# Optimization experiments

Measured on AMD Instinct MI355X. Metric: run time of the kernel, lower is better.

## Reference

```python
import jax, jax.numpy as jnp
import numpy as np

INPUT_DIM = 512
HIDDEN_DIM = 1024
OUTPUT_DIM = 1000
BATCH = 256
SEQ_LEN = 256


def setup_inputs() -> dict:
    key = jax.random.key(0)
    ks = jax.random.split(key, 7)
    std = 1.0 / np.sqrt(HIDDEN_DIM)
    u = lambda k, shape: jax.random.uniform(k, shape, jnp.float32, -std, std)
    return {
        "x": jax.random.normal(ks[0], (BATCH, SEQ_LEN, INPUT_DIM), jnp.float32),
        "w_x2h": u(ks[1], (4 * HIDDEN_DIM, INPUT_DIM)),
        "b_x2h": u(ks[2], (4 * HIDDEN_DIM,)),
        "w_h2h": u(ks[3], (4 * HIDDEN_DIM, HIDDEN_DIM)),
        "b_h2h": u(ks[4], (4 * HIDDEN_DIM,)),
        "w_fc": u(ks[5], (OUTPUT_DIM, HIDDEN_DIM)),
        "b_fc": u(ks[6], (OUTPUT_DIM,)),
    }


def _lstm_last_hidden(x, w_x2h, b_x2h, w_h2h, b_h2h):
    B, T, D = x.shape
    H = w_h2h.shape[1]
    # Precompute input-to-hidden for all timesteps in one big GEMM: [B,T,4H]
    xg = jnp.einsum("btd,gd->btg", x, w_x2h) + b_x2h + b_h2h
    xg = jnp.swapaxes(xg, 0, 1)  # [T,B,4H] for scan

    def step(carry, xg_t):
        h, c = carry
        gates = xg_t + h @ w_h2h.T  # [B,4H]
        i, f, g, o = jnp.split(gates, 4, axis=1)
        i = jax.nn.sigmoid(i)
        f = jax.nn.sigmoid(f)
        g = jnp.tanh(g)
        o = jax.nn.sigmoid(o)
        c = c * f + i * g
        h = o * jnp.tanh(c)
        return (h, c), None

    h0 = jnp.zeros((B, H), x.dtype)
    c0 = jnp.zeros((B, H), x.dtype)
    (h_last, _), _ = jax.lax.scan(step, (h0, c0), xg)
    return h_last


def reference(x, w_x2h, b_x2h, w_h2h, b_h2h, w_fc, b_fc):
    h_last = _lstm_last_hidden(x, w_x2h, b_x2h, w_h2h, b_h2h)  # [B,H]
    return h_last @ w_fc.T + b_fc  # [B,OUTPUT_DIM]
```

## Files before the change

kernel.cpp:

```cpp
#include <hip/hip_runtime.h>

typedef __attribute__((ext_vector_type(8))) short short8;
typedef __attribute__((ext_vector_type(4))) float floatx4;

#define DIN  512
#define HSZ  1024
#define G4   4096
#define KTOT 1536
#define BQ   256
#define TT   256

#define MFMA __builtin_amdgcn_mfma_f32_16x16x32_bf16

__device__ __forceinline__ unsigned short f2bf(float f){
  unsigned int u = __float_as_uint(f);
  u += 0x7fffu + ((u >> 16) & 1u);
  return (unsigned short)(u >> 16);
}
__device__ __forceinline__ unsigned int pack2(float a, float b){
  return (unsigned int)f2bf(a) | ((unsigned int)f2bf(b) << 16);
}

__global__ void prep_wcat(const float* __restrict__ wx, const float* __restrict__ wh,
                          const float* __restrict__ bx, const float* __restrict__ bh,
                          unsigned short* __restrict__ Wcat, float* __restrict__ bias){
  int gid = blockIdx.x * blockDim.x + threadIdx.x;
  int idx = gid * 8;
  int g = idx / KTOT;
  int k = idx - g * KTOT;
  const float* src = (k < DIN) ? (wx + (size_t)g * DIN + k)
                               : (wh + (size_t)g * HSZ + (k - DIN));
  float4 f0 = *(const float4*)(src);
  float4 f1 = *(const float4*)(src + 4);
  uint4 v = make_uint4(pack2(f0.x,f0.y), pack2(f0.z,f0.w), pack2(f1.x,f1.y), pack2(f1.z,f1.w));
  *(uint4*)(Wcat + (size_t)g * KTOT + k) = v;
  if (gid < G4) bias[gid] = bx[gid] + bh[gid];
}

__global__ void prep_wfc(const float* __restrict__ wfc, unsigned short* __restrict__ Wfcb){
  int gid = blockIdx.x * blockDim.x + threadIdx.x;
  int idx = gid * 8;
  int n = idx >> 10;
  int k = idx & 1023;
  uint4 v;
  if (n < 1000){
    const float* src = wfc + (size_t)n * 1024 + k;
    float4 f0 = *(const float4*)(src);
    float4 f1 = *(const float4*)(src + 4);
    v = make_uint4(pack2(f0.x,f0.y), pack2(f0.z,f0.w), pack2(f1.x,f1.y), pack2(f1.z,f1.w));
  } else {
    v = make_uint4(0u, 0u, 0u, 0u);
  }
  *(uint4*)(Wfcb + idx) = v;
}

__global__ void prep_x(const float* __restrict__ x, unsigned short* __restrict__ xbf){
  int gid = blockIdx.x * 256 + threadIdx.x;
  int d8 = gid & 63;
  int b  = (gid >> 6) & 255;
  int t  = gid >> 14;
  const float* src = x + (((size_t)b * TT) + t) * DIN + d8 * 8;
  float4 f0 = *(const float4*)(src);
  float4 f1 = *(const float4*)(src + 4);
  uint4 v = make_uint4(pack2(f0.x,f0.y), pack2(f0.z,f0.w), pack2(f1.x,f1.y), pack2(f1.z,f1.w));
  *(uint4*)(xbf + (((size_t)t * BQ) + b) * DIN + d8 * 8) = v;
}

__global__ void init_misc(unsigned int* __restrict__ h0w, unsigned int* __restrict__ cnt, int ncnt){
  int gid = blockIdx.x * 256 + threadIdx.x;
  if (gid < 131072) h0w[gid] = 0u;
  if (gid < ncnt)   cnt[gid] = 0u;
}

__global__ __launch_bounds__(512, 2)
void lstm_persist(const unsigned short* __restrict__ xbf,
                  const unsigned short* __restrict__ Wcat,
                  const float* __restrict__ bias,
                  unsigned short* __restrict__ hseq,
                  unsigned int* __restrict__ cnt){
  extern __shared__ char smem[];
  char*  Ws  = smem;
  float* Gt2 = (float*)(smem + 98304);
  float* Bls = (float*)(smem + 98304 + 34816);

  const int tid  = threadIdx.x;
  const int bx   = blockIdx.x;
  const int bg   = bx >> 7;
  const int b0   = bg << 7;
  const int u0   = (bx & 127) << 3;
  const int lane = tid & 63;
  const int w    = tid >> 6;
  const int rg   = w & 3;
  const int kg   = w >> 2;

  {
    int c  = tid >> 4;
    int ch = tid & 15;
    int g  = c >> 3, j = c & 7;
    const char* src = (const char*)(Wcat + (size_t)(g * HSZ + u0 + j) * KTOT);
    char* dst = Ws + c * 3072;
    int xr = j << 4;
    #pragma unroll
    for (int q = 0; q < 12; ++q){
      int k2 = ch * 192 + q * 16;
      *(uint4*)(dst + (k2 ^ xr)) = *(const uint4*)(src + k2);
    }
    if (tid < 32) Bls[tid] = bias[(size_t)(tid >> 3) * HSZ + u0 + (tid & 7)];
  }
  __syncthreads();

  const int kq8  = (lane >> 4) * 8;
  const int cA   = lane & 15;
  const int cB   = 16 + (lane & 15);
  const char* bpA = Ws + cA * 3072; const int xorA = (cA & 7) << 4;
  const char* bpB = Ws + cB * 3072; const int xorB = (cB & 7) << 4;

  const size_t rowA0 = (size_t)(b0 + rg * 32 + (lane & 15));

  const int erow = tid >> 2;
  const int eup  = (tid & 3) * 2;
  float cst0 = 0.f, cst1 = 0.f;

  for (int t = 0; t < TT; ++t){
    const unsigned short* hin  = hseq + (size_t)t * (BQ * HSZ);
    unsigned short*       hout = hseq + (size_t)(t + 1) * (BQ * HSZ);

    floatx4 acc[2][2][2];
    #pragma unroll
    for (int ab = 0; ab < 2; ++ab)
      #pragma unroll
      for (int rf = 0; rf < 2; ++rf)
        #pragma unroll
        for (int cf = 0; cf < 2; ++cf)
          acc[ab][rf][cf] = (floatx4){0.f,0.f,0.f,0.f};

    {
      const unsigned short* xr0 = xbf + ((size_t)t * BQ + rowA0) * DIN + kg * 256 + kq8;
      const unsigned short* xr1 = xr0 + (size_t)16 * DIN;
      const int bbase = kg * 512 + kq8 * 2;
      short8 a[4][2], b[4][2];
      #pragma unroll
      for (int p = 0; p < 4; ++p){
        a[p][0] = *(const short8*)(xr0 + p * 32);
        a[p][1] = *(const short8*)(xr1 + p * 32);
        int bb = bbase + p * 64;
        b[p][0] = *(const short8*)(bpA + (bb ^ xorA));
        b[p][1] = *(const short8*)(bpB + (bb ^ xorB));
      }
      #pragma unroll
      for (int j = 0; j < 8; ++j){
        int sl = j & 3, ab = j & 1;
        acc[ab][0][0] = MFMA(a[sl][0], b[sl][0], acc[ab][0][0], 0, 0, 0);
        acc[ab][0][1] = MFMA(a[sl][0], b[sl][1], acc[ab][0][1], 0, 0, 0);
        acc[ab][1][0] = MFMA(a[sl][1], b[sl][0], acc[ab][1][0], 0, 0, 0);
        acc[ab][1][1] = MFMA(a[sl][1], b[sl][1], acc[ab][1][1], 0, 0, 0);
        if (j < 4){
          int jj = j + 4;
          a[sl][0] = *(const short8*)(xr0 + jj * 32);
          a[sl][1] = *(const short8*)(xr1 + jj * 32);
          int bb = bbase + jj * 64;
          b[sl][0] = *(const short8*)(bpA + (bb ^ xorA));
          b[sl][1] = *(const short8*)(bpB + (bb ^ xorB));
        }
      }
    }

    if (t > 0){
      if (tid == 0){
        const unsigned int* cp = &cnt[((size_t)t * 2 + bg) * 32];
        while (__hip_atomic_load(cp, __ATOMIC_RELAXED, __HIP_MEMORY_SCOPE_AGENT) < 128u)
          __builtin_amdgcn_s_sleep(1);
      }
      __syncthreads();
      asm volatile("" ::: "memory");
    }

    {
      const unsigned short* hr0 = hin + rowA0 * HSZ + kg * 512 + kq8;
      const unsigned short* hr1 = hr0 + (size_t)16 * HSZ;
      const int bbase = 1024 + kg * 1024 + kq8 * 2;
      short8 a[4][2], b[4][2];
      #pragma unroll
      for (int p = 0; p < 4; ++p){
        a[p][0] = *(const short8*)(hr0 + p * 32);
        a[p][1] = *(const short8*)(hr1 + p * 32);
        int bb = bbase + p * 64;
        b[p][0] = *(const short8*)(bpA + (bb ^ xorA));
        b[p][1] = *(const short8*)(bpB + (bb ^ xorB));
      }
      #pragma unroll
      for (int j = 0; j < 16; ++j){
        int sl = j & 3, ab = j & 1;
        acc[ab][0][0] = MFMA(a[sl][0], b[sl][0], acc[ab][0][0], 0, 0, 0);
        acc[ab][0][1] = MFMA(a[sl][0], b[sl][1], acc[ab][0][1], 0, 0, 0);
        acc[ab][1][0] = MFMA(a[sl][1], b[sl][0], acc[ab][1][0], 0, 0, 0);
        acc[ab][1][1] = MFMA(a[sl][1], b[sl][1], acc[ab][1][1], 0, 0, 0);
        if (j < 12){
          int jj = j + 4;
          a[sl][0] = *(const short8*)(hr0 + jj * 32);
          a[sl][1] = *(const short8*)(hr1 + jj * 32);
          int bb = bbase + jj * 64;
          b[sl][0] = *(const short8*)(bpA + (bb ^ xorA));
          b[sl][1] = *(const short8*)(bpB + (bb ^ xorB));
        }
      }
    }

    {
      float* gdst = Gt2 + kg * (128 * 34);
      int r0 = rg * 32 + (lane >> 4) * 4;
      #pragma unroll
      for (int rf = 0; rf < 2; ++rf){
        floatx4 g0 = acc[0][rf][0] + acc[1][rf][0];
        floatx4 g1 = acc[0][rf][1] + acc[1][rf][1];
        #pragma unroll
        for (int r = 0; r < 4; ++r){
          gdst[(r0 + rf * 16 + r) * 34 + cA] = g0[r];
          gdst[(r0 + rf * 16 + r) * 34 + cB] = g1[r];
        }
      }
    }
    __syncthreads();

    {
      const float* g0p = Gt2 + erow * 34;
      const float* g1p = g0p + 128 * 34;
      float gi0 = g0p[     eup] + g1p[     eup] + Bls[     eup];
      float gf0 = g0p[ 8 + eup] + g1p[ 8 + eup] + Bls[ 8 + eup];
      float gg0 = g0p[16 + eup] + g1p[16 + eup] + Bls[16 + eup];
      float go0 = g0p[24 + eup] + g1p[24 + eup] + Bls[24 + eup];
      float gi1 = g0p[     eup + 1] + g1p[     eup + 1] + Bls[     eup + 1];
      float gf1 = g0p[ 8 + eup + 1] + g1p[ 8 + eup + 1] + Bls[ 8 + eup + 1];
      float gg1 = g0p[16 + eup + 1] + g1p[16 + eup + 1] + Bls[16 + eup + 1];
      float go1 = g0p[24 + eup + 1] + g1p[24 + eup + 1] + Bls[24 + eup + 1];

      float iv0 = 1.f / (1.f + __expf(-gi0));
      float fv0 = 1.f / (1.f + __expf(-gf0));
      float e20 = __expf(-2.f * fmaxf(fminf(gg0, 30.f), -30.f));
      float gv0 = (1.f - e20) / (1.f + e20);
      float ov0 = 1.f / (1.f + __expf(-go0));
      float cn0 = cst0 * fv0 + iv0 * gv0;
      cst0 = cn0;
      float ec0 = __expf(-2.f * fmaxf(fminf(cn0, 30.f), -30.f));
      float hv0 = ov0 * (1.f - ec0) / (1.f + ec0);

      float iv1 = 1.f / (1.f + __expf(-gi1));
      float fv1 = 1.f / (1.f + __expf(-gf1));
      float e21 = __expf(-2.f * fmaxf(fminf(gg1, 30.f), -30.f));
      float gv1 = (1.f - e21) / (1.f + e21);
      float ov1 = 1.f / (1.f + __expf(-go1));
      float cn1 = cst1 * fv1 + iv1 * gv1;
      cst1 = cn1;
      float ec1 = __expf(-2.f * fmaxf(fminf(cn1, 30.f), -30.f));
      float hv1 = ov1 * (1.f - ec1) / (1.f + ec1);

      __hip_atomic_store((unsigned int*)(hout + (size_t)(b0 + erow) * HSZ + u0 + eup),
                         pack2(hv0, hv1), __ATOMIC_RELAXED, __HIP_MEMORY_SCOPE_AGENT);
    }
    __syncthreads();

    if (tid == 0){
      __hip_atomic_fetch_add(&cnt[((size_t)(t + 1) * 2 + bg) * 32], 1u,
                             __ATOMIC_RELAXED, __HIP_MEMORY_SCOPE_AGENT);
    }
  }
}

__global__ __launch_bounds__(256, 1)
void fc_kernel(const unsigned short* __restrict__ h, const unsigned short* __restrict__ wfc,
               const float* __restrict__ bfc, float* __restrict__ out){
  int bx = blockIdx.x, tid = threadIdx.x;
  int wave = tid >> 6, lane = tid & 63;
  int row0 = (bx >> 4) * 64 + wave * 16;
  int col0 = (bx & 15) * 64;
  int lr = lane & 15, lk = (lane >> 4) * 8;
  floatx4 acc[4] = {{0.f,0.f,0.f,0.f},{0.f,0.f,0.f,0.f},{0.f,0.f,0.f,0.f},{0.f,0.f,0.f,0.f}};
  #pragma unroll 4
  for (int ks = 0; ks < 32; ++ks){
    int k = ks * 32 + lk;
    short8 a = *(const short8*)(h + (size_t)(row0 + lr) * 1024 + k);
    #pragma unroll
    for (int fj = 0; fj < 4; ++fj){
      short8 b = *(const short8*)(wfc + (size_t)(col0 + fj * 16 + lr) * 1024 + k);
      acc[fj] = MFMA(a, b, acc[fj], 0, 0, 0);
    }
  }
  #pragma unroll
  for (int fj = 0; fj < 4; ++fj){
    int col = col0 + fj * 16 + lr;
    if (col < 1000){
      #pragma unroll
      for (int r = 0; r < 4; ++r){
        int row = row0 + (lane >> 4) * 4 + r;
        out[(size_t)row * 1000 + col] = acc[fj][r] + bfc[col];
      }
    }
  }
}

extern "C" void kernel_launch(void* const* d_in, const int* in_sizes, int n_in,
                              void* d_out, int out_size, void* d_ws, size_t ws_size,
                              hipStream_t stream){
  const float* x    = (const float*)d_in[0];
  const float* wx2h = (const float*)d_in[1];
  const float* bx2h = (const float*)d_in[2];
  const float* wh2h = (const float*)d_in[3];
  const float* bh2h = (const float*)d_in[4];
  const float* wfc  = (const float*)d_in[5];
  const float* bfc  = (const float*)d_in[6];
  float* out = (float*)d_out;
  char* ws = (char*)d_ws;

  unsigned short* Wcat = (unsigned short*)(ws + 0);
  unsigned short* Wfcb = (unsigned short*)(ws + 12582912);
  float*          bias = (float*)         (ws + 14680064);
  unsigned short* xbf  = (unsigned short*)(ws + 14696448);
  unsigned short* hseq = (unsigned short*)(ws + 81805312);
  unsigned int*   cntb = (unsigned int*)  (ws + 216547328);

  (void)hipFuncSetAttribute((const void*)lstm_persist,
                            hipFuncAttributeMaxDynamicSharedMemorySize, 133376);

  hipLaunchKernelGGL(prep_wcat, dim3(3072), dim3(256), 0, stream, wx2h, wh2h, bx2h, bh2h, Wcat, bias);
  hipLaunchKernelGGL(prep_wfc,  dim3(512),  dim3(256), 0, stream, wfc, Wfcb);
  hipLaunchKernelGGL(prep_x,    dim3(16384),dim3(256), 0, stream, x, xbf);
  hipLaunchKernelGGL(init_misc, dim3(512),  dim3(256), 0, stream,
                     (unsigned int*)hseq, cntb, (int)(65792 / 4));

  hipLaunchKernelGGL(lstm_persist, dim3(256), dim3(512), 133376, stream,
                     xbf, Wcat, bias, hseq, cntb);

  hipLaunchKernelGGL(fc_kernel, dim3(64), dim3(256), 0, stream,
                     hseq + (size_t)256 * BQ * HSZ, Wfcb, bfc, out);
}
```

Before: 3.262 ms.

## Shard step barrier counters and hoist x/h loads around the wait

Splits each timestep's single 128-arrival counter into 8 sub-counters of 16 arrivals, each on its own cache line, and polls all 8 from one wavefront using a ballot. The aim is to reduce atomic contention on one address. The x-projection operand loads are now issued before the barrier so their latency overlaps the wait. The h-operand loads are all issued up front into 32 registers per wave, and LDS weight fragments are double-buffered. The added register pressure (X0/X1 plus A0/A1) may cause spills or lower occupancy, and the counter buffer is enlarged to match.

```diff
diff --git a/kernel.cpp b/kernel.cpp
--- a/kernel.cpp
+++ b/kernel.cpp
@@ -87,7 +87,8 @@
   const int bx   = blockIdx.x;
   const int bg   = bx >> 7;
   const int b0   = bg << 7;
-  const int u0   = (bx & 127) << 3;
+  const int hb   = bx & 127;
+  const int u0   = hb << 3;
   const int lane = tid & 63;
   const int w    = tid >> 6;
   const int rg   = w & 3;
@@ -134,75 +135,84 @@
         for (int cf = 0; cf < 2; ++cf)
           acc[ab][rf][cf] = (floatx4){0.f,0.f,0.f,0.f};
 
+    short8 X0[8], X1[8];
     {
       const unsigned short* xr0 = xbf + ((size_t)t * BQ + rowA0) * DIN + kg * 256 + kq8;
       const unsigned short* xr1 = xr0 + (size_t)16 * DIN;
-      const int bbase = kg * 512 + kq8 * 2;
-      short8 a[4][2], b[4][2];
-      #pragma unroll
-      for (int p = 0; p < 4; ++p){
-        a[p][0] = *(const short8*)(xr0 + p * 32);
-        a[p][1] = *(const short8*)(xr1 + p * 32);
-        int bb = bbase + p * 64;
-        b[p][0] = *(const short8*)(bpA + (bb ^ xorA));
-        b[p][1] = *(const short8*)(bpB + (bb ^ xorB));
-      }
-      #pragma unroll
-      for (int j = 0; j < 8; ++j){
-        int sl = j & 3, ab = j & 1;
-        acc[ab][0][0] = MFMA(a[sl][0], b[sl][0], acc[ab][0][0], 0, 0, 0);
-        acc[ab][0][1] = MFMA(a[sl][0], b[sl][1], acc[ab][0][1], 0, 0, 0);
-        acc[ab][1][0] = MFMA(a[sl][1], b[sl][0], acc[ab][1][0], 0, 0, 0);
-        acc[ab][1][1] = MFMA(a[sl][1], b[sl][1], acc[ab][1][1], 0, 0, 0);
-        if (j < 4){
-          int jj = j + 4;
-          a[sl][0] = *(const short8*)(xr0 + jj * 32);
-          a[sl][1] = *(const short8*)(xr1 + jj * 32);
-          int bb = bbase + jj * 64;
-          b[sl][0] = *(const short8*)(bpA + (bb ^ xorA));
-          b[sl][1] = *(const short8*)(bpB + (bb ^ xorB));
+      #pragma unroll
+      for (int p = 0; p < 8; ++p){
+        X0[p] = *(const short8*)(xr0 + p * 32);
+        X1[p] = *(const short8*)(xr1 + p * 32);
+      }
+    }
+    __builtin_amdgcn_sched_barrier(0);
+
+    if (t > 0){
+      if (tid < 64){
+        const unsigned int* cp = &cnt[(((size_t)t * 2 + bg) * 8) * 16];
+        const int g16 = (lane & 7) * 16;
+        while (true){
+          unsigned int v = __hip_atomic_load(cp + g16, __ATOMIC_RELAXED, __HIP_MEMORY_SCOPE_AGENT);
+          if (__ballot(v >= 16u) == ~0ull) break;
+          __builtin_amdgcn_s_sleep(1);
         }
-      }
-    }
-
-    if (t > 0){
-      if (tid == 0){
-        const unsigned int* cp = &cnt[((size_t)t * 2 + bg) * 32];
-        while (__hip_atomic_load(cp, __ATOMIC_RELAXED, __HIP_MEMORY_SCOPE_AGENT) < 128u)
-          __builtin_amdgcn_s_sleep(1);
       }
       __syncthreads();
       asm volatile("" ::: "memory");
     }
 
     {
+      const int bbase = kg * 512 + kq8 * 2;
+      short8 bA[2], bB[2];
+      bA[0] = *(const short8*)(bpA + ((bbase     ) ^ xorA));
+      bB[0] = *(const short8*)(bpB + ((bbase     ) ^ xorB));
+      bA[1] = *(const short8*)(bpA + ((bbase + 64) ^ xorA));
+      bB[1] = *(const short8*)(bpB + ((bbase + 64) ^ xorB));
+      #pragma unroll
+      for (int j = 0; j < 8; ++j){
+        const int sl = j & 1;
+        short8 b0 = bA[sl], b1 = bB[sl];
+        if (j < 6){
+          int bb = bbase + (j + 2) * 64;
+          bA[sl] = *(const short8*)(bpA + (bb ^ xorA));
+          bB[sl] = *(const short8*)(bpB + (bb ^ xorB));
+        }
+        acc[sl][0][0] = MFMA(X0[j], b0, acc[sl][0][0], 0, 0, 0);
+        acc[sl][0][1] = MFMA(X0[j], b1, acc[sl][0][1], 0, 0, 0);
+        acc[sl][1][0] = MFMA(X1[j], b0, acc[sl][1][0], 0, 0, 0);
+        acc[sl][1][1] = MFMA(X1[j], b1, acc[sl][1][1], 0, 0, 0);
+      }
+    }
+
+    {
       const unsigned short* hr0 = hin + rowA0 * HSZ + kg * 512 + kq8;
       const unsigned short* hr1 = hr0 + (size_t)16 * HSZ;
+      short8 A0[16], A1[16];
+      #pragma unroll
+      for (int p = 0; p < 16; ++p){
+        A0[p] = *(const short8*)(hr0 + p * 32);
+        A1[p] = *(const short8*)(hr1 + p * 32);
+      }
+      __builtin_amdgcn_sched_barrier(0);
       const int bbase = 1024 + kg * 1024 + kq8 * 2;
-      short8 a[4][2], b[4][2];
-      #pragma unroll
-      for (int p = 0; p < 4; ++p){
-        a[p][0] = *(const short8*)(hr0 + p * 32);
-        a[p][1] = *(const short8*)(hr1 + p * 32);
-        int bb = bbase + p * 64;
-        b[p][0] = *(const short8*)(bpA + (bb ^ xorA));
-        b[p][1] = *(const short8*)(bpB + (bb ^ xorB));
-      }
+      short8 bA[2], bB[2];
+      bA[0] = *(const short8*)(bpA + ((bbase     ) ^ xorA));
+      bB[0] = *(const short8*)(bpB + ((bbase     ) ^ xorB));
+      bA[1] = *(const short8*)(bpA + ((bbase + 64) ^ xorA));
+      bB[1] = *(const short8*)(bpB + ((bbase + 64) ^ xorB));
       #pragma unroll
       for (int j = 0; j < 16; ++j){
-        int sl = j & 3, ab = j & 1;
-        acc[ab][0][0] = MFMA(a[sl][0], b[sl][0], acc[ab][0][0], 0, 0, 0);
-        acc[ab][0][1] = MFMA(a[sl][0], b[sl][1], acc[ab][0][1], 0, 0, 0);
-        acc[ab][1][0] = MFMA(a[sl][1], b[sl][0], acc[ab][1][0], 0, 0, 0);
-        acc[ab][1][1] = MFMA(a[sl][1], b[sl][1], acc[ab][1][1], 0, 0, 0);
-        if (j < 12){
-          int jj = j + 4;
-          a[sl][0] = *(const short8*)(hr0 + jj * 32);
-          a[sl][1] = *(const short8*)(hr1 + jj * 32);
-          int bb = bbase + jj * 64;
-          b[sl][0] = *(const short8*)(bpA + (bb ^ xorA));
-          b[sl][1] = *(const short8*)(bpB + (bb ^ xorB));
+        const int sl = j & 1;
+        short8 b0 = bA[sl], b1 = bB[sl];
+        if (j < 14){
+          int bb = bbase + (j + 2) * 64;
+          bA[sl] = *(const short8*)(bpA + (bb ^ xorA));
+          bB[sl] = *(const short8*)(bpB + (bb ^ xorB));
         }
+        acc[sl][0][0] = MFMA(A0[j], b0, acc[sl][0][0], 0, 0, 0);
+        acc[sl][0][1] = MFMA(A0[j], b1, acc[sl][0][1], 0, 0, 0);
+        acc[sl][1][0] = MFMA(A1[j], b0, acc[sl][1][0], 0, 0, 0);
+        acc[sl][1][1] = MFMA(A1[j], b1, acc[sl][1][1], 0, 0, 0);
       }
     }
 
@@ -260,7 +270,7 @@
     __syncthreads();
 
     if (tid == 0){
-      __hip_atomic_fetch_add(&cnt[((size_t)(t + 1) * 2 + bg) * 32], 1u,
+      __hip_atomic_fetch_add(&cnt[(((size_t)(t + 1) * 2 + bg) * 8 + (hb >> 4)) * 16], 1u,
                              __ATOMIC_RELAXED, __HIP_MEMORY_SCOPE_AGENT);
     }
   }
@@ -325,7 +335,7 @@
   hipLaunchKernelGGL(prep_wfc,  dim3(512),  dim3(256), 0, stream, wfc, Wfcb);
   hipLaunchKernelGGL(prep_x,    dim3(16384),dim3(256), 0, stream, x, xbf);
   hipLaunchKernelGGL(init_misc, dim3(512),  dim3(256), 0, stream,
-                     (unsigned int*)hseq, cntb, (int)(65792 / 4));
+                     (unsigned int*)hseq, cntb, (int)(263168 / 4));
 
   hipLaunchKernelGGL(lstm_persist, dim3(256), dim3(512), 133376, stream,
                      xbf, Wcat, bias, hseq, cntb);
```

After: 3.109 ms. -4.7%, faster.
